# Kernel tuning notes

Measured on AMD Instinct MI355X. Metric: run time of the kernel, lower is better.

Reference implementation:

```python
import jax, jax.numpy as jnp
import numpy as np

N, E, D, ED, FD, H, Q, K, G = 50000, 600000, 128, 128, 512, 1, 3, 512, 512
NEG_SLOPE = 0.2
EPS = 1e-5


def setup_inputs() -> dict:
    key = jax.random.key(0)
    ks = jax.random.split(key, 16)
    inp = {
        'x': jax.random.normal(ks[0], (N, D), jnp.float32),
        'edge_index': jax.random.randint(ks[1], (2, E), 0, N, jnp.int32),
        'edge_attr': jax.random.normal(ks[2], (E, ED), jnp.float32),
        'batch_vec': jnp.sort(jax.random.randint(ks[3], (N,), 0, G, jnp.int32)),
        'W_l': jax.random.normal(ks[4], (D, H * D), jnp.float32),
        'b_l': jnp.zeros((H * D,), jnp.float32),
        'W_r': jax.random.normal(ks[5], (D, H * D), jnp.float32),
        'b_r': jnp.zeros((H * D,), jnp.float32),
        'W_edge': jax.random.normal(ks[6], (ED, H * D), jnp.float32),
        'att': jax.random.normal(ks[7], (H, D), jnp.float32),
        'conv_bias': jnp.zeros((H * D,), jnp.float32),
        'adapter_W': jax.random.normal(ks[8], (D, D), jnp.float32),
        'adapter_b': jnp.zeros((D,), jnp.float32),
        'norm_g': jnp.ones((D,), jnp.float32),
        'norm_b': jnp.zeros((D,), jnp.float32),
        'codebooks': jax.random.normal(ks[9], (Q, K, D), jnp.float32),
        'out_W': jax.random.normal(ks[10], (D, FD), jnp.float32),
        'out_b': jnp.zeros((FD,), jnp.float32),
        'outnorm_g': jnp.ones((FD,), jnp.float32),
        'outnorm_b': jnp.zeros((FD,), jnp.float32),
    }
    return inp


def _layer_norm(x, g, b):
    m = x.mean(-1, keepdims=True)
    v = ((x - m) ** 2).mean(-1, keepdims=True)
    return (x - m) * jax.lax.rsqrt(v + EPS) * g + b


def _forward(x, edge_index, edge_attr, batch_vec, W_l, b_l, W_r, b_r, W_edge, att,
             conv_bias, adapter_W, adapter_b, norm_g, norm_b, codebooks, out_W, out_b,
             outnorm_g, outnorm_b):
    sg = jax.lax.stop_gradient
    n = x.shape[0]
    # ---- GATv2Conv (PyG defaults: add_self_loops=True, fill_value='mean') ----
    loops = jnp.arange(n, dtype=edge_index.dtype)
    src = jnp.concatenate([edge_index[0], loops])
    dst = jnp.concatenate([edge_index[1], loops])
    mean_attr = edge_attr.mean(0)
    ea = jnp.concatenate([edge_attr, jnp.broadcast_to(mean_attr, (n, edge_attr.shape[1]))])
    xl = (x @ W_l + b_l).reshape(n, H, D)   # source transform
    xr = (x @ W_r + b_r).reshape(n, H, D)   # target transform
    e_emb = (ea @ W_edge).reshape(-1, H, D)
    e = xl[src] + xr[dst] + e_emb           # [Etot,H,D]
    score = jnp.einsum('ehd,hd->eh', jax.nn.leaky_relu(e, NEG_SLOPE), att)
    smax = jax.ops.segment_max(score, dst, num_segments=n)
    ex = jnp.exp(score - smax[dst])
    denom = jax.ops.segment_sum(ex, dst, num_segments=n)
    alpha = ex / (denom[dst] + 1e-16)       # per-target softmax
    out = jax.ops.segment_sum(xl[src] * alpha[..., None], dst, num_segments=n)  # [n,H,D]
    out = out.reshape(n, H * D) + conv_bias
    h = out.reshape(n, H, D).mean(1)        # mean over heads
    # ---- global mean pool over graphs ----
    sums = jax.ops.segment_sum(h, batch_vec, num_segments=G)
    cnts = jax.ops.segment_sum(jnp.ones((n,), h.dtype), batch_vec, num_segments=G)
    g = sums / jnp.maximum(cnts, 1.0)[:, None]
    # ---- adapter + layernorm ----
    g = g @ adapter_W + adapter_b
    g = _layer_norm(g, norm_g, norm_b)
    # ---- residual VQ (euclidean nearest code, straight-through) ----
    residual = g
    quantized_out = jnp.zeros_like(g)
    codes, idxs, commits = [], [], []
    cb_sq = (codebooks ** 2).sum(-1)        # [Q,K]
    for q in range(Q):
        cb = codebooks[q]
        d2 = (residual ** 2).sum(-1, keepdims=True) - 2.0 * residual @ cb.T + cb_sq[q]
        idx = jnp.argmin(d2, axis=-1)
        code = cb[idx]
        commits.append(((sg(code) - residual) ** 2).mean())
        quantized_out = quantized_out + residual + sg(code - residual)
        codes.append(code)
        idxs.append(idx)
        residual = residual - sg(code)
    commit_loss = jnp.stack(commits).mean()
    residual_loss = ((g - quantized_out) ** 2).mean()
    loss = commit_loss + residual_loss
    indices = jnp.stack(idxs, axis=1)       # [G,Q]
    # ---- per-quantizer straight-through tokens -> projection -> layernorm ----
    tokens = jnp.stack([g + sg(c - g) for c in codes], axis=1)  # [G,Q,D]
    tokens = tokens @ out_W + out_b                              # [G,Q,FD]
    tokens = _layer_norm(tokens, outnorm_g, outnorm_b)
    return tokens, indices, loss


def reference(x, edge_index, edge_attr, batch_vec, W_l, b_l, W_r, b_r, W_edge, att,
              conv_bias, adapter_W, adapter_b, norm_g, norm_b, codebooks, out_W, out_b,
              outnorm_g, outnorm_b):
    return _forward(x, edge_index, edge_attr, batch_vec, W_l, b_l, W_r, b_r, W_edge,
                    att, conv_bias, adapter_W, adapter_b, norm_g, norm_b, codebooks,
                    out_W, out_b, outnorm_g, outnorm_b)
```

## Files before the change

kernel.cpp:

```cpp
#include <hip/hip_runtime.h>
#include <math.h>

#define N_NODES 50000
#define E_EDGES 600000
#define DD 128
#define G_GRAPHS 512
#define K_CODES 512
#define Q_QUANT 3
#define FD_OUT 512
#define NEG_SLOPE 0.2f
#define LN_EPS 1e-5f

static __device__ __forceinline__ float lrelu(float v){ return v > 0.f ? v : NEG_SLOPE*v; }
static __device__ __forceinline__ float wsum(float v){
#pragma unroll
  for (int m = 1; m < 64; m <<= 1) v += __shfl_xor(v, m);
  return v;
}
static __device__ __forceinline__ float wmax(float v){
#pragma unroll
  for (int m = 1; m < 64; m <<= 1) v = fmaxf(v, __shfl_xor(v, m));
  return v;
}

#define EA_LD 130

__global__ __launch_bounds__(256)
void k_xform2(const float* __restrict__ x,
              const float* __restrict__ W_l, const float* __restrict__ b_l,
              const float* __restrict__ W_r, const float* __restrict__ b_r,
              float* __restrict__ xl, float* __restrict__ xr, int n)
{
  __shared__ __align__(16) float xt[64*EA_LD];
  __shared__ __align__(16) float WtL[32*128];
  __shared__ __align__(16) float WtR[32*128];
  const int tid = threadIdx.x;
  const int r0 = blockIdx.x * 64;
  {
    const int q = tid & 63, eb = tid >> 6;
#pragma unroll
    for (int i = 0; i < 16; ++i){
      int e = eb + 4*i;
      int row = r0 + e;
      float2 v = make_float2(0.f, 0.f);
      if (row < n) v = *(const float2*)&x[row*DD + q*2];
      *(float2*)&xt[e*EA_LD + q*2] = v;
    }
  }
  const int eg = tid >> 4;
  const int cg = tid & 15;
  float accL[4][8], accR[4][8];
#pragma unroll
  for (int j = 0; j < 4; ++j)
#pragma unroll
    for (int u = 0; u < 8; ++u){ accL[j][u] = 0.f; accR[j][u] = 0.f; }

  for (int kq = 0; kq < 4; ++kq){
    __syncthreads();
    {
      const int c4 = tid & 31, kb = tid >> 5;
#pragma unroll
      for (int i = 0; i < 4; ++i){
        int kk = kb + 8*i;
        *(float4*)&WtL[kk*128 + c4*4] = *(const float4*)&W_l[(kq*32+kk)*DD + c4*4];
        *(float4*)&WtR[kk*128 + c4*4] = *(const float4*)&W_r[(kq*32+kk)*DD + c4*4];
      }
    }
    __syncthreads();
    const int kb2 = kq*32;
#pragma unroll 4
    for (int k = 0; k < 32; ++k){
      float aa[4];
#pragma unroll
      for (int j = 0; j < 4; ++j) aa[j] = xt[(eg*4+j)*EA_LD + kb2 + k];
      float bL[8], bR[8];
      *(float4*)&bL[0] = *(const float4*)&WtL[k*128 + cg*4];
      *(float4*)&bL[4] = *(const float4*)&WtL[k*128 + 64 + cg*4];
      *(float4*)&bR[0] = *(const float4*)&WtR[k*128 + cg*4];
      *(float4*)&bR[4] = *(const float4*)&WtR[k*128 + 64 + cg*4];
#pragma unroll
      for (int j = 0; j < 4; ++j){
#pragma unroll
        for (int u = 0; u < 8; ++u) accL[j][u] = fmaf(aa[j], bL[u], accL[j][u]);
#pragma unroll
        for (int u = 0; u < 8; ++u) accR[j][u] = fmaf(aa[j], bR[u], accR[j][u]);
      }
    }
  }
  float bvL[8], bvR[8];
  *(float4*)&bvL[0] = *(const float4*)&b_l[cg*4];
  *(float4*)&bvL[4] = *(const float4*)&b_l[64 + cg*4];
  *(float4*)&bvR[0] = *(const float4*)&b_r[cg*4];
  *(float4*)&bvR[4] = *(const float4*)&b_r[64 + cg*4];
#pragma unroll
  for (int j = 0; j < 4; ++j){
    int row = r0 + eg*4 + j;
    if (row < n){
      float oL[8], oR[8];
#pragma unroll
      for (int u = 0; u < 8; ++u){ oL[u] = accL[j][u] + bvL[u]; oR[u] = accR[j][u] + bvR[u]; }
      *(float4*)&xl[row*DD + cg*4]      = *(const float4*)&oL[0];
      *(float4*)&xl[row*DD + 64 + cg*4] = *(const float4*)&oL[4];
      *(float4*)&xr[row*DD + cg*4]      = *(const float4*)&oR[0];
      *(float4*)&xr[row*DD + 64 + cg*4] = *(const float4*)&oR[4];
    }
  }
}

__global__ __launch_bounds__(256)
void k_edge(const float* __restrict__ edge_attr, const float* __restrict__ W_edge,
            const int* __restrict__ ei, const float* __restrict__ xl,
            const float* __restrict__ xr, const float* __restrict__ att,
            const int* __restrict__ off, int* __restrict__ pos,
            uint2* __restrict__ rec, float* __restrict__ asum_mid)
{
  __shared__ __align__(16) float ea[64*EA_LD];
  __shared__ __align__(16) float Wt[32*128];
  const int tid = threadIdx.x;
  const int e0 = blockIdx.x * 64;
  {
    const int q = tid & 63, eb = tid >> 6;
#pragma unroll
    for (int i = 0; i < 16; ++i){
      int e = eb + 4*i;
      *(float2*)&ea[e*EA_LD + q*2] = *(const float2*)&edge_attr[(e0+e)*DD + q*2];
    }
  }
  const int eg = tid >> 4;
  const int cg = tid & 15;
  float acc[4][8];
#pragma unroll
  for (int j = 0; j < 4; ++j)
#pragma unroll
    for (int u = 0; u < 8; ++u) acc[j][u] = 0.f;

  for (int kq = 0; kq < 4; ++kq){
    __syncthreads();
    {
      const int c4 = tid & 31, kb = tid >> 5;
#pragma unroll
      for (int i = 0; i < 4; ++i){
        int kk = kb + 8*i;
        *(float4*)&Wt[kk*128 + c4*4] = *(const float4*)&W_edge[(kq*32+kk)*DD + c4*4];
      }
    }
    __syncthreads();
    const int kb2 = kq*32;
#pragma unroll 4
    for (int k = 0; k < 32; ++k){
      float aa[4];
#pragma unroll
      for (int j = 0; j < 4; ++j) aa[j] = ea[(eg*4+j)*EA_LD + kb2 + k];
      float bb[8];
      *(float4*)&bb[0] = *(const float4*)&Wt[k*128 + cg*4];
      *(float4*)&bb[4] = *(const float4*)&Wt[k*128 + 64 + cg*4];
#pragma unroll
      for (int j = 0; j < 4; ++j)
#pragma unroll
        for (int u = 0; u < 8; ++u) acc[j][u] = fmaf(aa[j], bb[u], acc[j][u]);
    }
  }
  float attv[8];
  *(float4*)&attv[0] = *(const float4*)&att[cg*4];
  *(float4*)&attv[4] = *(const float4*)&att[64 + cg*4];
  float sp[4];
  int dsts[4], srcs[4];
#pragma unroll
  for (int j = 0; j < 4; ++j){
    int e = e0 + eg*4 + j;
    int s = ei[e];
    int d = ei[E_EDGES + e];
    srcs[j] = s; dsts[j] = d;
    float xlv[8], xrv[8];
    *(float4*)&xlv[0] = *(const float4*)&xl[s*DD + cg*4];
    *(float4*)&xlv[4] = *(const float4*)&xl[s*DD + 64 + cg*4];
    *(float4*)&xrv[0] = *(const float4*)&xr[d*DD + cg*4];
    *(float4*)&xrv[4] = *(const float4*)&xr[d*DD + 64 + cg*4];
    float p = 0.f;
#pragma unroll
    for (int u = 0; u < 8; ++u){
      float vv = acc[j][u] + xlv[u] + xrv[u];
      p += lrelu(vv) * attv[u];
    }
    sp[j] = p;
  }
#pragma unroll
  for (int m = 1; m < 16; m <<= 1){
#pragma unroll
    for (int j = 0; j < 4; ++j) sp[j] += __shfl_xor(sp[j], m);
  }
  if (cg == 0){
#pragma unroll
    for (int j = 0; j < 4; ++j){
      int d = dsts[j];
      int p = atomicAdd(&pos[d], 1);
      uint2 r;
      r.x = (unsigned)srcs[j];
      r.y = __float_as_uint(sp[j]);
      rec[off[d] + p] = r;
    }
  }
  if (tid < 128){
    float s = 0.f;
    for (int e = 0; e < 64; ++e) s += ea[e*EA_LD + tid];
    atomicAdd(&asum_mid[(blockIdx.x & 63)*DD + tid], s);
  }
}

__global__ __launch_bounds__(128)
void k_me(const float* __restrict__ asum_mid, const float* __restrict__ W_edge,
          float* __restrict__ me)
{
  __shared__ float mean[128];
  const int d = threadIdx.x;
  float s = 0.f;
  for (int r = 0; r < 64; ++r) s += asum_mid[r*DD + d];
  mean[d] = s / (float)E_EDGES;
  __syncthreads();
  float acc = 0.f;
  for (int k = 0; k < 128; ++k) acc += mean[k] * W_edge[k*DD + d];
  me[d] = acc;
}

__global__ __launch_bounds__(256)
void k_hist(const int* __restrict__ ei, int* __restrict__ indeg)
{
  int e = blockIdx.x*256 + threadIdx.x;
  if (e < E_EDGES) atomicAdd(&indeg[ei[E_EDGES + e]], 1);
}

#define SC_NB ((N_NODES + 511) / 512)
__global__ __launch_bounds__(512)
void k_scan1(const int* __restrict__ indeg, int* __restrict__ off, int* __restrict__ bsum)
{
  __shared__ int s[512];
  const int tid = threadIdx.x;
  const int gid = blockIdx.x*512 + tid;
  int v = (gid < N_NODES) ? indeg[gid] : 0;
  s[tid] = v;
  __syncthreads();
  for (int d = 1; d < 512; d <<= 1){
    int t = (tid >= d) ? s[tid-d] : 0;
    __syncthreads();
    s[tid] += t;
    __syncthreads();
  }
  if (gid < N_NODES) off[gid] = s[tid] - v;
  if (tid == 511) bsum[blockIdx.x] = s[511];
}

__global__ __launch_bounds__(128)
void k_scan2(const int* __restrict__ bsum, int* __restrict__ boff)
{
  __shared__ int s[128];
  const int tid = threadIdx.x;
  int v = (tid < SC_NB) ? bsum[tid] : 0;
  s[tid] = v;
  __syncthreads();
  for (int d = 1; d < 128; d <<= 1){
    int t = (tid >= d) ? s[tid-d] : 0;
    __syncthreads();
    s[tid] += t;
    __syncthreads();
  }
  if (tid < SC_NB) boff[tid] = s[tid] - v;
}

__global__ __launch_bounds__(512)
void k_scan3(int* __restrict__ off, const int* __restrict__ boff)
{
  const int gid = blockIdx.x*512 + threadIdx.x;
  if (gid < N_NODES) off[gid] += boff[blockIdx.x];
  if (gid == 0) off[N_NODES] = E_EDGES;
}

__global__ __launch_bounds__(256)
void k_aggregate(const int* __restrict__ off, const uint2* __restrict__ rec,
                 const float* __restrict__ xl, const float* __restrict__ xr,
                 const float* __restrict__ me, const float* __restrict__ att,
                 const float* __restrict__ conv_bias, const int* __restrict__ batch_vec,
                 float* __restrict__ gsum, float* __restrict__ gcnt)
{
  __shared__ float hshare[4][128];
  __shared__ int bsh[4];
  const int tid = threadIdx.x, lane = tid & 63, wid = tid >> 6;
  const int i = blockIdx.x*4 + wid;
  float2 xli = *(const float2*)&xl[i*DD + lane*2];
  float2 xri = *(const float2*)&xr[i*DD + lane*2];
  float2 mev = *(const float2*)&me[lane*2];
  float2 attv = *(const float2*)&att[lane*2];
  float v0 = xli.x + xri.x + mev.x;
  float v1 = xli.y + xri.y + mev.y;
  float s_self = wsum(lrelu(v0)*attv.x + lrelu(v1)*attv.y);
  const int o0 = off[i], o1 = off[i+1];
  const int deg = o1 - o0;
  uint2 myrec = make_uint2(0u, __float_as_uint(-INFINITY));
  float m = s_self;
  if (lane < deg) myrec = rec[o0 + lane];
  m = fmaxf(m, __uint_as_float(myrec.y));
  for (int b = 64; b < deg; b += 64){
    int j = b + lane;
    if (j < deg) m = fmaxf(m, __uint_as_float(rec[o0 + j].y));
  }
  m = wmax(m);
  float wse = __expf(s_self - m);
  float den = wse;
  float a0 = wse * xli.x, a1 = wse * xli.y;
  if (deg <= 64){
    float msc = __uint_as_float(myrec.y);
    int msrc = (int)myrec.x;
#pragma unroll 4
    for (int j = 0; j < deg; ++j){
      float sc = __shfl(msc, j);
      int s = __shfl(msrc, j);
      float w = __expf(sc - m);
      den += w;
      float2 xs = *(const float2*)&xl[s*DD + lane*2];
      a0 = fmaf(w, xs.x, a0);
      a1 = fmaf(w, xs.y, a1);
    }
  } else {
#pragma unroll 4
    for (int j = 0; j < deg; ++j){
      uint2 r = rec[o0 + j];
      float w = __expf(__uint_as_float(r.y) - m);
      den += w;
      float2 xs = *(const float2*)&xl[(int)r.x*DD + lane*2];
      a0 = fmaf(w, xs.x, a0);
      a1 = fmaf(w, xs.y, a1);
    }
  }
  float inv = 1.0f / (den + 1e-16f);
  float2 cb2 = *(const float2*)&conv_bias[lane*2];
  float h0 = a0*inv + cb2.x;
  float h1 = a1*inv + cb2.y;
  int b = batch_vec[i];
  hshare[wid][lane*2]     = h0;
  hshare[wid][lane*2 + 1] = h1;
  if (lane == 0) bsh[wid] = b;
  __syncthreads();
  bool uni = (bsh[0]==bsh[1]) && (bsh[1]==bsh[2]) && (bsh[2]==bsh[3]);
  if (uni){
    if (wid == 0){
      float s0 = hshare[0][lane*2] + hshare[1][lane*2] + hshare[2][lane*2] + hshare[3][lane*2];
      float s1 = hshare[0][lane*2+1] + hshare[1][lane*2+1] + hshare[2][lane*2+1] + hshare[3][lane*2+1];
      atomicAdd(&gsum[b*DD + lane*2],     s0);
      atomicAdd(&gsum[b*DD + lane*2 + 1], s1);
      if (lane == 0) atomicAdd(&gcnt[b], 4.0f);
    }
  } else {
    atomicAdd(&gsum[b*DD + lane*2],     h0);
    atomicAdd(&gsum[b*DD + lane*2 + 1], h1);
    if (lane == 0) atomicAdd(&gcnt[b], 1.0f);
  }
}

__global__ __launch_bounds__(128)
void k_pool(const float* __restrict__ gsum, const float* __restrict__ gcnt,
            const float* __restrict__ aW, const float* __restrict__ ab,
            const float* __restrict__ ng, const float* __restrict__ nb,
            float* __restrict__ g_ln)
{
  __shared__ float row[128];
  __shared__ float red[128];
  const int g = blockIdx.x, d = threadIdx.x;
  float denom = fmaxf(gcnt[g], 1.0f);
  row[d] = gsum[g*DD + d] / denom;
  __syncthreads();
  double accd = (double)ab[d];
  for (int k = 0; k < 128; ++k) accd += (double)row[k] * (double)aW[k*DD + d];
  float a = (float)accd;
  red[d] = a; __syncthreads();
  for (int s = 64; s > 0; s >>= 1){ if (d < s) red[d] += red[d+s]; __syncthreads(); }
  float mean = red[0] / 128.f; __syncthreads();
  float c = a - mean;
  red[d] = c*c; __syncthreads();
  for (int s = 64; s > 0; s >>= 1){ if (d < s) red[d] += red[d+s]; __syncthreads(); }
  float var = red[0] / 128.f; __syncthreads();
  float inv = (float)(1.0 / sqrt((double)var + (double)LN_EPS));
  g_ln[g*DD + d] = c * inv * ng[d] + nb[d];
}

__global__ __launch_bounds__(256)
void k_rvq(const float* __restrict__ g_ln, const float* __restrict__ codebooks,
           float* __restrict__ ind_out, int* __restrict__ idx_i,
           float* __restrict__ accs)
{
  __shared__ __align__(16) float r_lds[128];
  __shared__ float red[128];
  __shared__ double bd[64];
  __shared__ int bi[64];
  __shared__ int chosen;
  const int g = blockIdx.x, tid = threadIdx.x;
  if (tid < 128) r_lds[tid] = g_ln[g*DD + tid];
  __syncthreads();
  const int cl = tid >> 2, dq = tid & 3;
  for (int q = 0; q < Q_QUANT; ++q){
    const float* cb = codebooks + (size_t)q * K_CODES * DD;
    double bestd = 1e300; int besti = 1 << 30;
    for (int r = 0; r < 8; ++r){
      int c = r*64 + cl;
      double rc = 0.0, cc = 0.0;
      const float4* cp = (const float4*)&cb[c*DD + dq*32];
      const float4* rp = (const float4*)&r_lds[dq*32];
#pragma unroll
      for (int i = 0; i < 8; ++i){
        float4 cv = cp[i]; float4 rv = rp[i];
        rc += (double)cv.x*rv.x + (double)cv.y*rv.y + (double)cv.z*rv.z + (double)cv.w*rv.w;
        cc += (double)cv.x*cv.x + (double)cv.y*cv.y + (double)cv.z*cv.z + (double)cv.w*cv.w;
      }
      rc += __shfl_xor(rc, 1); rc += __shfl_xor(rc, 2);
      cc += __shfl_xor(cc, 1); cc += __shfl_xor(cc, 2);
      if (dq == 0){
        double d2 = cc - 2.0*rc;
        if (d2 < bestd || (d2 == bestd && c < besti)){ bestd = d2; besti = c; }
      }
    }
    if (dq == 0){ bd[cl] = bestd; bi[cl] = besti; }
    __syncthreads();
    if (tid < 64){
      double d2 = bd[tid]; int ii = bi[tid];
#pragma unroll
      for (int m = 1; m < 64; m <<= 1){
        double od = __shfl_xor(d2, m); int oi = __shfl_xor(ii, m);
        if (od < d2 || (od == d2 && oi < ii)){ d2 = od; ii = oi; }
      }
      if (tid == 0) chosen = ii;
    }
    __syncthreads();
    const int idx = chosen;
    if (tid == 0){
      ind_out[g*Q_QUANT + q] = (float)idx;
      idx_i[g*Q_QUANT + q] = idx;
    }
    if (tid < 128){
      float cd = cb[idx*DD + tid];
      float diff = cd - r_lds[tid];
      red[tid] = diff * diff;
      r_lds[tid] -= cd;
    }
    __syncthreads();
    for (int s = 64; s > 0; s >>= 1){ if (tid < s) red[tid] += red[tid+s]; __syncthreads(); }
    if (tid == 0) atomicAdd(&accs[q], red[0]);
    __syncthreads();
  }
  if (tid < 128) red[tid] = r_lds[tid]*r_lds[tid];
  __syncthreads();
  for (int s = 64; s > 0; s >>= 1){ if (tid < s) red[tid] += red[tid+s]; __syncthreads(); }
  if (tid == 0) atomicAdd(&accs[3], red[0]);
}

__global__ __launch_bounds__(256)
void k_tokens(const float* __restrict__ codebooks, const int* __restrict__ idx_i,
              const float* __restrict__ out_W, const float* __restrict__ out_b,
              const float* __restrict__ og, const float* __restrict__ ob,
              float* __restrict__ tokens)
{
  __shared__ __align__(16) float c_lds[128];
  __shared__ float red[256];
  const int blk = blockIdx.x;
  const int g = blk / 3, q = blk % 3;
  const int tid = threadIdx.x;
  const int idx = idx_i[g*Q_QUANT + q];
  if (tid < 128) c_lds[tid] = codebooks[((size_t)q*K_CODES + idx)*DD + tid];
  __syncthreads();
  double v0 = (double)out_b[tid];
  double v1 = (double)out_b[tid + 256];
  for (int k = 0; k < 128; ++k){
    double ck = (double)c_lds[k];
    v0 += ck * (double)out_W[k*FD_OUT + tid];
    v1 += ck * (double)out_W[k*FD_OUT + tid + 256];
  }
  float f0 = (float)v0, f1 = (float)v1;
  red[tid] = f0 + f1; __syncthreads();
  for (int s = 128; s > 0; s >>= 1){ if (tid < s) red[tid] += red[tid+s]; __syncthreads(); }
  float mean = red[0] / 512.f; __syncthreads();
  float d0 = f0 - mean, d1 = f1 - mean;
  red[tid] = d0*d0 + d1*d1; __syncthreads();
  for (int s = 128; s > 0; s >>= 1){ if (tid < s) red[tid] += red[tid+s]; __syncthreads(); }
  float var = red[0] / 512.f; __syncthreads();
  float inv = (float)(1.0 / sqrt((double)var + (double)LN_EPS));
  tokens[(size_t)blk*FD_OUT + tid]       = d0*inv*og[tid] + ob[tid];
  tokens[(size_t)blk*FD_OUT + tid + 256] = d1*inv*og[tid+256] + ob[tid+256];
}

__global__ void k_loss(const float* __restrict__ accs, float* __restrict__ out)
{
  float commit = (accs[0] + accs[1] + accs[2]) / (3.0f * G_GRAPHS * DD);
  float resid  = accs[3] / ((float)G_GRAPHS * DD);
  out[0] = commit + resid;
}

extern "C" void kernel_launch(void* const* d_in, const int* in_sizes, int n_in,
                              void* d_out, int out_size, void* d_ws, size_t ws_size,
                              hipStream_t stream)
{
  (void)in_sizes; (void)n_in; (void)out_size; (void)ws_size;
  const float* x         = (const float*)d_in[0];
  const int*   ei        = (const int*)d_in[1];
  const float* edge_attr = (const float*)d_in[2];
  const int*   batch_vec = (const int*)d_in[3];
  const float* W_l       = (const float*)d_in[4];
  const float* b_l       = (const float*)d_in[5];
  const float* W_r       = (const float*)d_in[6];
  const float* b_r       = (const float*)d_in[7];
  const float* W_edge    = (const float*)d_in[8];
  const float* att       = (const float*)d_in[9];
  const float* conv_bias = (const float*)d_in[10];
  const float* aW        = (const float*)d_in[11];
  const float* ab        = (const float*)d_in[12];
  const float* ng        = (const float*)d_in[13];
  const float* nb        = (const float*)d_in[14];
  const float* codebooks = (const float*)d_in[15];
  const float* out_W     = (const float*)d_in[16];
  const float* out_b     = (const float*)d_in[17];
  const float* og        = (const float*)d_in[18];
  const float* ob        = (const float*)d_in[19];
  float* outf = (float*)d_out;

  char* w = (char*)d_ws;
  size_t o = 0;
  auto nxt = [&](size_t bytes)->void*{
    void* p = w + o;
    o += (bytes + 511) & ~(size_t)511;
    return p;
  };
  int*   indeg    = (int*)  nxt((size_t)N_NODES*4);
  int*   pos      = (int*)  nxt((size_t)N_NODES*4);
  float* asum_mid = (float*)nxt((size_t)64*DD*4);
  float* gsum     = (float*)nxt((size_t)G_GRAPHS*DD*4);
  float* gcnt     = (float*)nxt((size_t)G_GRAPHS*4);
  float* accs     = (float*)nxt(16);
  const size_t zero_span = o;
  int*   off      = (int*)  nxt((size_t)(N_NODES+1)*4);
  float* xl       = (float*)nxt((size_t)N_NODES*DD*4);
  float* xr       = (float*)nxt((size_t)N_NODES*DD*4);
  uint2* rec      = (uint2*)nxt((size_t)E_EDGES*8);
  float* me       = (float*)nxt((size_t)DD*4);
  float* g_ln     = (float*)nxt((size_t)G_GRAPHS*DD*4);
  int*   idx_i    = (int*)  nxt((size_t)G_GRAPHS*Q_QUANT*4);
  int*   bsum     = (int*)  nxt((size_t)SC_NB*4);
  int*   boff     = (int*)  nxt((size_t)SC_NB*4);

  hipMemsetAsync(w, 0, zero_span, stream);

  k_hist<<<dim3((E_EDGES+255)/256), dim3(256), 0, stream>>>(ei, indeg);
  k_scan1<<<dim3(SC_NB), dim3(512), 0, stream>>>(indeg, off, bsum);
  k_scan2<<<dim3(1), dim3(128), 0, stream>>>(bsum, boff);
  k_scan3<<<dim3(SC_NB), dim3(512), 0, stream>>>(off, boff);
  k_xform2<<<dim3((N_NODES+63)/64), dim3(256), 0, stream>>>(x, W_l, b_l, W_r, b_r,
                                                            xl, xr, N_NODES);
  k_edge<<<dim3(E_EDGES/64), dim3(256), 0, stream>>>(edge_attr, W_edge, ei, xl, xr, att,
                                                     off, pos, rec, asum_mid);
  k_me<<<dim3(1), dim3(128), 0, stream>>>(asum_mid, W_edge, me);
  k_aggregate<<<dim3(N_NODES/4), dim3(256), 0, stream>>>(off, rec, xl, xr, me, att,
                                                         conv_bias, batch_vec, gsum, gcnt);
  k_pool<<<dim3(G_GRAPHS), dim3(128), 0, stream>>>(gsum, gcnt, aW, ab, ng, nb, g_ln);
  k_rvq<<<dim3(G_GRAPHS), dim3(256), 0, stream>>>(g_ln, codebooks,
                                                  outf + (size_t)G_GRAPHS*Q_QUANT*FD_OUT,
                                                  idx_i, accs);
  k_tokens<<<dim3(G_GRAPHS*Q_QUANT), dim3(256), 0, stream>>>(codebooks, idx_i, out_W, out_b,
                                                             og, ob, outf);
  k_loss<<<dim3(1), dim3(1), 0, stream>>>(accs,
                                          outf + (size_t)G_GRAPHS*Q_QUANT*FD_OUT
                                               + (size_t)G_GRAPHS*Q_QUANT);
}
```

Baseline: 580.5 us.

## Use split-bf16 MFMA for edge projection GEMM in edge kernel

Replaces the FP32 FMA edge_attr×W_edge GEMM in the edge kernel with bf16 MFMA 16x16x32 instructions. It keeps near-FP32 accuracy by splitting each operand into high and low bf16 parts and doing three products (hh, hl, lh). A small pre-kernel splits and transposes W_edge into bf16 hi/lo arrays. The gathered xl[src]+xr[dst] sums are staged in shared memory to match the MFMA output layout, and the column-sum for the mean attribute now uses wave shuffles. The aim is to cut VALU-bound GEMM time. The costs are a slight accuracy change and extra conversion work.

```diff
diff --git a/kernel.cpp b/kernel.cpp
--- a/kernel.cpp
+++ b/kernel.cpp
@@ -11,6 +11,9 @@
 #define NEG_SLOPE 0.2f
 #define LN_EPS 1e-5f
 
+using short8 = __attribute__((ext_vector_type(8))) short;
+using f32x4  = __attribute__((ext_vector_type(4))) float;
+
 static __device__ __forceinline__ float lrelu(float v){ return v > 0.f ? v : NEG_SLOPE*v; }
 static __device__ __forceinline__ float wsum(float v){
 #pragma unroll
@@ -21,6 +24,14 @@
 #pragma unroll
   for (int m = 1; m < 64; m <<= 1) v = fmaxf(v, __shfl_xor(v, m));
   return v;
+}
+static __device__ __forceinline__ ushort f2bf(float f){
+  unsigned u = __float_as_uint(f);
+  unsigned r = (u + 0x7fffu + ((u >> 16) & 1u)) >> 16;
+  return (ushort)r;
+}
+static __device__ __forceinline__ float bf2f(ushort s){
+  return __uint_as_float(((unsigned)s) << 16);
 }
 
 #define EA_LD 130
@@ -107,103 +118,150 @@
   }
 }
 
+__global__ __launch_bounds__(128)
+void k_wsplit(const float* __restrict__ W, ushort* __restrict__ Wbh, ushort* __restrict__ Wbl)
+{
+  const int n = blockIdx.x;
+  const int k = threadIdx.x;
+  float v = W[k*DD + n];
+  ushort h = f2bf(v);
+  Wbh[n*DD + k] = h;
+  Wbl[n*DD + k] = f2bf(v - bf2f(h));
+}
+
+#define AP 40
+#define WP 40
+#define XSP 132
+
 __global__ __launch_bounds__(256)
-void k_edge(const float* __restrict__ edge_attr, const float* __restrict__ W_edge,
+void k_edge(const float* __restrict__ edge_attr,
+            const ushort* __restrict__ Wbh, const ushort* __restrict__ Wbl,
             const int* __restrict__ ei, const float* __restrict__ xl,
             const float* __restrict__ xr, const float* __restrict__ att,
             const int* __restrict__ off, int* __restrict__ pos,
             uint2* __restrict__ rec, float* __restrict__ asum_mid)
 {
-  __shared__ __align__(16) float ea[64*EA_LD];
-  __shared__ __align__(16) float Wt[32*128];
+  __shared__ __align__(16) char smem[64*XSP*4];
+  ushort* Ah = (ushort*)smem;
+  ushort* Al = (ushort*)(smem + 5120);
+  ushort* Wh = (ushort*)(smem + 10240);
+  ushort* Wl = (ushort*)(smem + 20480);
+  float*  xs = (float*)smem;
+
   const int tid = threadIdx.x;
+  const int w = tid >> 6, lane = tid & 63;
   const int e0 = blockIdx.x * 64;
+
+  const int ar  = tid & 63;
+  const int ak  = w * 8;
+  const int wn  = tid & 127;
+  const int wk2 = (tid >> 7) * 16;
+
+  const int mrow = w * 16 + (lane & 15);
+  const int koff = (lane >> 4) * 8;
+  const int nrow = lane & 15;
+
+  f32x4 acc[8];
+#pragma unroll
+  for (int nt = 0; nt < 8; ++nt){ f32x4 z = {0.f,0.f,0.f,0.f}; acc[nt] = z; }
+
+  for (int kq = 0; kq < 4; ++kq){
+    if (kq) __syncthreads();
+    float av[8];
+    *(float4*)&av[0] = *(const float4*)&edge_attr[(size_t)(e0+ar)*DD + kq*32 + ak];
+    *(float4*)&av[4] = *(const float4*)&edge_attr[(size_t)(e0+ar)*DD + kq*32 + ak + 4];
+    short8 vh, vl;
+#pragma unroll
+    for (int i = 0; i < 8; ++i){
+      ushort h = f2bf(av[i]);
+      vh[i] = (short)h;
+      vl[i] = (short)f2bf(av[i] - bf2f(h));
+    }
+    *(short8*)&Ah[ar*AP + ak] = vh;
+    *(short8*)&Al[ar*AP + ak] = vl;
+    {
+      float cs[8];
+#pragma unroll
+      for (int i = 0; i < 8; ++i) cs[i] = av[i];
+#pragma unroll
+      for (int m = 1; m < 64; m <<= 1){
+#pragma unroll
+        for (int i = 0; i < 8; ++i) cs[i] += __shfl_xor(cs[i], m);
+      }
+      if (lane == 0){
+#pragma unroll
+        for (int i = 0; i < 8; ++i)
+          atomicAdd(&asum_mid[(blockIdx.x & 63)*DD + kq*32 + ak + i], cs[i]);
+      }
+    }
+    {
+      const ushort* gh = &Wbh[wn*DD + kq*32 + wk2];
+      const ushort* gl = &Wbl[wn*DD + kq*32 + wk2];
+      *(short8*)&Wh[wn*WP + wk2]     = *(const short8*)&gh[0];
+      *(short8*)&Wh[wn*WP + wk2 + 8] = *(const short8*)&gh[8];
+      *(short8*)&Wl[wn*WP + wk2]     = *(const short8*)&gl[0];
+      *(short8*)&Wl[wn*WP + wk2 + 8] = *(const short8*)&gl[8];
+    }
+    __syncthreads();
+    short8 a_h = *(const short8*)&Ah[mrow*AP + koff];
+    short8 a_l = *(const short8*)&Al[mrow*AP + koff];
+    short8 bh[8];
+#pragma unroll
+    for (int nt = 0; nt < 8; ++nt)
+      bh[nt] = *(const short8*)&Wh[(nt*16 + nrow)*WP + koff];
+#pragma unroll
+    for (int nt = 0; nt < 8; ++nt)
+      acc[nt] = __builtin_amdgcn_mfma_f32_16x16x32_bf16(a_h, bh[nt], acc[nt], 0, 0, 0);
+#pragma unroll
+    for (int nt = 0; nt < 8; ++nt){
+      short8 bl = *(const short8*)&Wl[(nt*16 + nrow)*WP + koff];
+      acc[nt] = __builtin_amdgcn_mfma_f32_16x16x32_bf16(a_h, bl, acc[nt], 0, 0, 0);
+    }
+#pragma unroll
+    for (int nt = 0; nt < 8; ++nt)
+      acc[nt] = __builtin_amdgcn_mfma_f32_16x16x32_bf16(a_l, bh[nt], acc[nt], 0, 0, 0);
+  }
+  __syncthreads();
   {
-    const int q = tid & 63, eb = tid >> 6;
-#pragma unroll
-    for (int i = 0; i < 16; ++i){
-      int e = eb + 4*i;
-      *(float2*)&ea[e*EA_LD + q*2] = *(const float2*)&edge_attr[(e0+e)*DD + q*2];
-    }
-  }
-  const int eg = tid >> 4;
-  const int cg = tid & 15;
-  float acc[4][8];
-#pragma unroll
-  for (int j = 0; j < 4; ++j)
-#pragma unroll
-    for (int u = 0; u < 8; ++u) acc[j][u] = 0.f;
-
-  for (int kq = 0; kq < 4; ++kq){
-    __syncthreads();
-    {
-      const int c4 = tid & 31, kb = tid >> 5;
-#pragma unroll
-      for (int i = 0; i < 4; ++i){
-        int kk = kb + 8*i;
-        *(float4*)&Wt[kk*128 + c4*4] = *(const float4*)&W_edge[(kq*32+kk)*DD + c4*4];
-      }
-    }
-    __syncthreads();
-    const int kb2 = kq*32;
-#pragma unroll 4
-    for (int k = 0; k < 32; ++k){
-      float aa[4];
-#pragma unroll
-      for (int j = 0; j < 4; ++j) aa[j] = ea[(eg*4+j)*EA_LD + kb2 + k];
-      float bb[8];
-      *(float4*)&bb[0] = *(const float4*)&Wt[k*128 + cg*4];
-      *(float4*)&bb[4] = *(const float4*)&Wt[k*128 + 64 + cg*4];
-#pragma unroll
-      for (int j = 0; j < 4; ++j)
-#pragma unroll
-        for (int u = 0; u < 8; ++u) acc[j][u] = fmaf(aa[j], bb[u], acc[j][u]);
-    }
-  }
+    const int s0 = ei[e0 + ar];
+    const int d0 = ei[E_EDGES + e0 + ar];
+    const int cc = w * 32;
+#pragma unroll
+    for (int i = 0; i < 8; ++i){
+      float4 a = *(const float4*)&xl[(size_t)s0*DD + cc + i*4];
+      float4 b = *(const float4*)&xr[(size_t)d0*DD + cc + i*4];
+      *(float4*)&xs[ar*XSP + cc + i*4] = make_float4(a.x+b.x, a.y+b.y, a.z+b.z, a.w+b.w);
+    }
+  }
+  __syncthreads();
   float attv[8];
-  *(float4*)&attv[0] = *(const float4*)&att[cg*4];
-  *(float4*)&attv[4] = *(const float4*)&att[64 + cg*4];
-  float sp[4];
-  int dsts[4], srcs[4];
-#pragma unroll
-  for (int j = 0; j < 4; ++j){
-    int e = e0 + eg*4 + j;
-    int s = ei[e];
-    int d = ei[E_EDGES + e];
-    srcs[j] = s; dsts[j] = d;
-    float xlv[8], xrv[8];
-    *(float4*)&xlv[0] = *(const float4*)&xl[s*DD + cg*4];
-    *(float4*)&xlv[4] = *(const float4*)&xl[s*DD + 64 + cg*4];
-    *(float4*)&xrv[0] = *(const float4*)&xr[d*DD + cg*4];
-    *(float4*)&xrv[4] = *(const float4*)&xr[d*DD + 64 + cg*4];
-    float p = 0.f;
-#pragma unroll
-    for (int u = 0; u < 8; ++u){
-      float vv = acc[j][u] + xlv[u] + xrv[u];
-      p += lrelu(vv) * attv[u];
-    }
-    sp[j] = p;
+#pragma unroll
+  for (int nt = 0; nt < 8; ++nt) attv[nt] = att[nt*16 + nrow];
+  float p[4] = {0.f, 0.f, 0.f, 0.f};
+  const int rb = w*16 + (lane >> 4)*4;
+#pragma unroll
+  for (int nt = 0; nt < 8; ++nt){
+#pragma unroll
+    for (int j = 0; j < 4; ++j){
+      float ev = acc[nt][j] + xs[(rb + j)*XSP + nt*16 + nrow];
+      p[j] += lrelu(ev) * attv[nt];
+    }
   }
 #pragma unroll
   for (int m = 1; m < 16; m <<= 1){
 #pragma unroll
-    for (int j = 0; j < 4; ++j) sp[j] += __shfl_xor(sp[j], m);
-  }
-  if (cg == 0){
+    for (int j = 0; j < 4; ++j) p[j] += __shfl_xor(p[j], m);
+  }
+  if ((lane & 15) == 0){
 #pragma unroll
     for (int j = 0; j < 4; ++j){
-      int d = dsts[j];
-      int p = atomicAdd(&pos[d], 1);
-      uint2 r;
-      r.x = (unsigned)srcs[j];
-      r.y = __float_as_uint(sp[j]);
-      rec[off[d] + p] = r;
-    }
-  }
-  if (tid < 128){
-    float s = 0.f;
-    for (int e = 0; e < 64; ++e) s += ea[e*EA_LD + tid];
-    atomicAdd(&asum_mid[(blockIdx.x & 63)*DD + tid], s);
+      int e = e0 + rb + j;
+      int d = ei[E_EDGES + e];
+      int s = ei[e];
+      int pp = atomicAdd(&pos[d], 1);
+      uint2 r; r.x = (unsigned)s; r.y = __float_as_uint(p[j]);
+      rec[off[d] + pp] = r;
+    }
   }
 }
 
@@ -541,16 +599,19 @@
   int*   idx_i    = (int*)  nxt((size_t)G_GRAPHS*Q_QUANT*4);
   int*   bsum     = (int*)  nxt((size_t)SC_NB*4);
   int*   boff     = (int*)  nxt((size_t)SC_NB*4);
+  ushort* Wbh     = (ushort*)nxt((size_t)DD*DD*2);
+  ushort* Wbl     = (ushort*)nxt((size_t)DD*DD*2);
 
   hipMemsetAsync(w, 0, zero_span, stream);
 
+  k_wsplit<<<dim3(128), dim3(128), 0, stream>>>(W_edge, Wbh, Wbl);
   k_hist<<<dim3((E_EDGES+255)/256), dim3(256), 0, stream>>>(ei, indeg);
   k_scan1<<<dim3(SC_NB), dim3(512), 0, stream>>>(indeg, off, bsum);
   k_scan2<<<dim3(1), dim3(128), 0, stream>>>(bsum, boff);
   k_scan3<<<dim3(SC_NB), dim3(512), 0, stream>>>(off, boff);
   k_xform2<<<dim3((N_NODES+63)/64), dim3(256), 0, stream>>>(x, W_l, b_l, W_r, b_r,
                                                             xl, xr, N_NODES);
-  k_edge<<<dim3(E_EDGES/64), dim3(256), 0, stream>>>(edge_attr, W_edge, ei, xl, xr, att,
+  k_edge<<<dim3(E_EDGES/64), dim3(256), 0, stream>>>(edge_attr, Wbh, Wbl, ei, xl, xr, att,
                                                      off, pos, rec, asum_mid);
   k_me<<<dim3(1), dim3(128), 0, stream>>>(asum_mid, W_edge, me);
   k_aggregate<<<dim3(N_NODES/4), dim3(256), 0, stream>>>(off, rec, xl, xr, me, att,
```

New measurement: 606.8 us. 4.5% more time.
